# Optimization experiments

Hardware: AMD Instinct MI355X
Metric: run time of the kernel (lower is better)

The kernel has to match this reference:

```python
import jax, jax.numpy as jnp
import numpy as np

B, N, D, H, E, ED = 32, 256, 1024, 16, 512, 256
HD = D // H
NEG = float(np.finfo(np.float32).min)


def setup_inputs() -> dict:
    key = jax.random.key(0)
    ks = iter(jax.random.split(key, 16))
    def nrm(shape, fan_in):
        return jax.random.normal(next(ks), shape, jnp.float32) / np.sqrt(fan_in)
    return {
        "x": jax.random.normal(next(ks), (B, N, D), jnp.float32),
        "node_masks": jnp.ones((B, N), jnp.float32),
        "relation_edges": jax.random.randint(next(ks), (B, E, 2), 0, N, jnp.int64),
        "relation_masks": jnp.ones((B, E), jnp.float32),
        "relation_embeddings": jax.random.normal(next(ks), (B, E, ED), jnp.float32),
        "ln_g": jnp.ones((D,), jnp.float32), "ln_b": jnp.zeros((D,), jnp.float32),
        "Wq": nrm((D, D), D), "bq": jnp.zeros((D,), jnp.float32),
        "Wk": nrm((D, D), D), "bk": jnp.zeros((D,), jnp.float32),
        "Wv": nrm((D, D), D), "bv": jnp.zeros((D,), jnp.float32),
        "We": nrm((ED, H), ED), "be": jnp.zeros((H,), jnp.float32),
        "Wo": nrm((D, D), D), "bo": jnp.zeros((D,), jnp.float32),
        "ff_g": jnp.ones((D,), jnp.float32), "ff_b": jnp.zeros((D,), jnp.float32),
        "W1": nrm((D, 4 * D), D), "b1": jnp.zeros((4 * D,), jnp.float32),
        "W2": nrm((4 * D, D), 4 * D), "b2": jnp.zeros((D,), jnp.float32),
    }


def _ln(x, g, b):
    m = jnp.mean(x, axis=-1, keepdims=True)
    v = jnp.mean((x - m) ** 2, axis=-1, keepdims=True)
    return (x - m) / jnp.sqrt(v + 1e-5) * g + b


def reference(x, node_masks, relation_edges, relation_masks, relation_embeddings,
              ln_g, ln_b, Wq, bq, Wk, bk, Wv, bv, We, be, Wo, bo,
              ff_g, ff_b, W1, b1, W2, b2):
    residual = x
    xn = _ln(x, ln_g, ln_b)
    # [B,N,D] -> [B,H,N,HD]
    def split_heads(t):
        return t.reshape(B, N, H, HD).transpose(0, 2, 1, 3)
    q = split_heads(xn @ Wq + bq)
    k = split_heads(xn @ Wk + bk)
    v = split_heads(xn @ Wv + bv)
    attn = jnp.einsum('bhqd,bhkd->bhqk', q, k) / np.sqrt(HD)

    nb = node_masks.astype(bool)
    pair_mask = nb[:, None, :, None] & nb[:, None, None, :]  # [B,1,N,N]

    # --- scatter edge list into dense adjacency + per-head bias ---
    src = jnp.clip(relation_edges[..., 0], 0, N - 1)  # [B,E]
    dst = jnp.clip(relation_edges[..., 1], 0, N - 1)
    valid = relation_masks.astype(bool)
    # route invalid edges to a padding row/col N, sliced off afterwards
    src_w = jnp.where(valid, src, N)
    dst_w = jnp.where(valid, dst, N)
    b_idx = jnp.broadcast_to(jnp.arange(B)[:, None], (B, E))

    Np = N + 1
    adj = jnp.broadcast_to(jnp.eye(Np, dtype=bool), (B, Np, Np))
    adj = adj.at[b_idx, src_w, dst_w].set(True).at[b_idx, dst_w, src_w].set(True)
    rel_adj = adj[:, :N, :N][:, None]  # [B,1,N,N]

    eb = relation_embeddings @ We + be  # [B,E,H]
    bias = jnp.zeros((B, Np, Np, H), x.dtype)
    bias = bias.at[b_idx, src_w, dst_w].set(eb).at[b_idx, dst_w, src_w].set(eb)
    rel_bias = bias[:, :N, :N, :].transpose(0, 3, 1, 2)  # [B,H,N,N]

    attn = attn + rel_bias
    pair_mask = pair_mask & rel_adj
    attn = jnp.where(pair_mask, attn, NEG)
    attn = jax.nn.softmax(attn, axis=-1)
    attn = jnp.nan_to_num(attn)

    out = jnp.einsum('bhqk,bhkd->bhqd', attn, v).transpose(0, 2, 1, 3).reshape(B, N, D)
    x = residual + (out @ Wo + bo)
    h = _ln(x, ff_g, ff_b)
    h = jax.nn.silu(h @ W1 + b1) @ W2 + b2
    x = x + h
    return x * node_masks[..., None]
```

## Files before the change

kernel.cpp:

```cpp
#include <hip/hip_runtime.h>
#include <math.h>

#define B_  32
#define N_  256
#define D_  1024
#define H_  16
#define E_  512
#define ED_ 256
#define HD_ 64
#define QS_ 3072
#define NEG_ (-3.4028234663852886e38f)

typedef __attribute__((ext_vector_type(8))) short short8;
typedef __attribute__((ext_vector_type(4))) float f32x4;
typedef __attribute__((ext_vector_type(16))) float f32x16;
typedef unsigned short ushort_t;
typedef unsigned int uint_t;

union U16x8 { uint4 u4; ushort_t s[8]; };

static __device__ __forceinline__ ushort_t f2bf(float f) {
    uint_t u = __builtin_bit_cast(uint_t, f);
    u = (u + 0x7fff + ((u >> 16) & 1)) >> 16;
    return (ushort_t)u;
}

static __device__ __forceinline__ void gload_lds16(const void* g, void* l) {
    __builtin_amdgcn_global_load_lds(
        (const __attribute__((address_space(1))) unsigned int*)g,
        (__attribute__((address_space(3))) unsigned int*)l, 16, 0, 0);
}

__global__ __launch_bounds__(256) void ln_bf16_kernel(const float* __restrict__ x,
                                                      const float* __restrict__ g,
                                                      const float* __restrict__ b,
                                                      ushort_t* __restrict__ out) {
    int row = blockIdx.x;
    const float* xr = x + (size_t)row * D_;
    ushort_t* yr = out + (size_t)row * D_;
    __shared__ float red[256];
    int t = threadIdx.x;
    float vals[4];
    float s = 0.f;
#pragma unroll
    for (int i = 0; i < 4; ++i) { vals[i] = xr[t + i * 256]; s += vals[i]; }
    red[t] = s; __syncthreads();
    for (int off = 128; off > 0; off >>= 1) { if (t < off) red[t] += red[t + off]; __syncthreads(); }
    float mean = red[0] * (1.f / D_);
    __syncthreads();
    float vs = 0.f;
#pragma unroll
    for (int i = 0; i < 4; ++i) { float d = vals[i] - mean; vs += d * d; }
    red[t] = vs; __syncthreads();
    for (int off = 128; off > 0; off >>= 1) { if (t < off) red[t] += red[t + off]; __syncthreads(); }
    float rstd = 1.f / sqrtf(red[0] * (1.f / D_) + 1e-5f);
#pragma unroll
    for (int i = 0; i < 4; ++i) {
        int c = t + i * 256;
        yr[c] = f2bf((vals[i] - mean) * rstd * g[c] + b[c]);
    }
}

__global__ __launch_bounds__(256) void prep_kernel(
    const float* __restrict__ Wq, const float* __restrict__ Wk,
    const float* __restrict__ Wv, const float* __restrict__ Wo,
    const float* __restrict__ W1, const float* __restrict__ W2,
    const float* __restrict__ bq, const float* __restrict__ bk,
    const float* __restrict__ bv,
    ushort_t* __restrict__ qkvT, ushort_t* __restrict__ WoT,
    ushort_t* __restrict__ W1T, ushort_t* __restrict__ W2T,
    float* __restrict__ cb)
{
    int id = blockIdx.x;
    if (id >= 12288) {
        int i = (id - 12288) * 256 + threadIdx.x;
        cb[i] = (i < 1024) ? bq[i] : ((i < 2048) ? bk[i - 1024] : bv[i - 2048]);
        return;
    }
    const float* in; ushort_t* outp; int K, N, tid;
    if (id < 4096) {
        int wsel = id >> 10; tid = id & 1023; K = D_; N = D_;
        in   = (wsel == 0) ? Wq : (wsel == 1) ? Wk : (wsel == 2) ? Wv : Wo;
        outp = (wsel == 0) ? qkvT : (wsel == 1) ? qkvT + 1024 * 1024
             : (wsel == 2) ? qkvT + 2 * 1024 * 1024 : WoT;
    } else if (id < 8192) { tid = id - 4096; K = D_; N = 4 * D_; in = W1; outp = W1T; }
    else                  { tid = id - 8192; K = 4 * D_; N = D_; in = W2; outp = W2T; }
    int tilesX = N >> 5;
    int n0 = (tid % tilesX) * 32, k0 = (tid / tilesX) * 32;

    __shared__ float tile[32][33];
    int tx = threadIdx.x & 31, ty = threadIdx.x >> 5;
#pragma unroll
    for (int r = 0; r < 4; ++r)
        tile[ty + r * 8][tx] = in[(size_t)(k0 + ty + r * 8) * N + n0 + tx];
    __syncthreads();
#pragma unroll
    for (int r = 0; r < 4; ++r)
        outp[(size_t)(n0 + ty + r * 8) * K + k0 + tx] = f2bf(tile[tx][ty + r * 8]);
}

__global__ __launch_bounds__(256) void eb_kernel(const float* __restrict__ re,
                                                 const float* __restrict__ We,
                                                 const float* __restrict__ be,
                                                 float* __restrict__ eb) {
    __shared__ float rs[16 * 256];
    __shared__ float wl[256 * 16];
    int t = threadIdx.x;
    int be0 = blockIdx.x * 16;
#pragma unroll
    for (int i = 0; i < 16; ++i) wl[t + i * 256] = We[t + i * 256];
#pragma unroll
    for (int i = 0; i < 16; ++i) rs[t + i * 256] = re[(size_t)be0 * 256 + t + i * 256];
    __syncthreads();
    int el = t >> 4, h = t & 15;
    float s = be[h];
#pragma unroll 8
    for (int i = 0; i < 256; ++i) s += rs[el * 256 + i] * wl[i * 16 + h];
    eb[(size_t)(be0 + el) * 16 + h] = s;
}

__global__ void scatter_kernel(const int* __restrict__ edges, const float* __restrict__ emask,
                               int* __restrict__ prio) {
    int idx = blockIdx.x * blockDim.x + threadIdx.x;
    if (idx >= B_ * E_) return;
    if (emask[idx] == 0.f) return;
    int b = idx / E_, e = idx % E_;
    int s = edges[2 * idx], d = edges[2 * idx + 1];
    s = min(max(s, 0), N_ - 1);
    d = min(max(d, 0), N_ - 1);
    int* base = prio + (size_t)b * N_ * N_;
    atomicMax(&base[s * N_ + d], e);
    atomicMax(&base[d * N_ + s], e + E_);
}

template<int MODE>
__global__ __launch_bounds__(256) void gemm_bf16(
    const ushort_t* __restrict__ A, const ushort_t* __restrict__ BT,
    const float* __restrict__ bias, const float* __restrict__ res,
    const float* __restrict__ nm, void* __restrict__ Cout,
    int M, int N, int K)
{
    __shared__ ushort_t As[128 * 64];
    __shared__ ushort_t Bs[128 * 64];
    int t = threadIdx.x;
    int lane = t & 63;
    int l31 = lane & 31, lh = lane >> 5;
    int w = t >> 6;
    int wr = (w >> 1) * 64, wc = (w & 1) * 64;

    int bid = blockIdx.x;
    int xcd = bid & 7;
    int lid = bid >> 3;
    int st  = lid >> 5;
    int ls  = lid & 31;
    int brow = xcd * 8 + (ls >> 2);
    int bcol = st * 4 + (ls & 3);
    int row0 = brow * 128, col0 = bcol * 128;

    const ushort_t* Ag = A + (size_t)row0 * K;
    const ushort_t* Bg = BT + (size_t)col0 * K;
    int srow = t >> 3;
    int slot = t & 7;
    int sc = (slot ^ (srow & 7)) * 8;

    f32x16 acc[2][2];
#pragma unroll
    for (int i = 0; i < 2; ++i)
#pragma unroll
        for (int j = 0; j < 2; ++j)
#pragma unroll
            for (int r = 0; r < 16; ++r) acc[i][j][r] = 0.f;

    for (int k0 = 0; k0 < K; k0 += 64) {
#pragma unroll
        for (int i = 0; i < 4; ++i) {
            gload_lds16(Ag + (size_t)(i * 32 + srow) * K + k0 + sc, (char*)As + i * 4096 + t * 16);
            gload_lds16(Bg + (size_t)(i * 32 + srow) * K + k0 + sc, (char*)Bs + i * 4096 + t * 16);
        }
        __syncthreads();
#pragma unroll
        for (int ks = 0; ks < 4; ++ks) {
            short8 af[2], bf[2];
#pragma unroll
            for (int it = 0; it < 2; ++it) {
                int m = wr + it * 32 + l31;
                int x = ((ks * 2 + lh) ^ (m & 7)) * 16;
                af[it] = *(const short8*)((const char*)As + m * 128 + x);
            }
#pragma unroll
            for (int jt = 0; jt < 2; ++jt) {
                int n = wc + jt * 32 + l31;
                int x = ((ks * 2 + lh) ^ (n & 7)) * 16;
                bf[jt] = *(const short8*)((const char*)Bs + n * 128 + x);
            }
#pragma unroll
            for (int it = 0; it < 2; ++it)
#pragma unroll
                for (int jt = 0; jt < 2; ++jt)
                    acc[it][jt] = __builtin_amdgcn_mfma_f32_32x32x16_bf16(af[it], bf[jt], acc[it][jt], 0, 0, 0);
        }
        __syncthreads();
    }

#pragma unroll
    for (int it = 0; it < 2; ++it) {
#pragma unroll
        for (int jt = 0; jt < 2; ++jt) {
            int col = col0 + wc + jt * 32 + l31;
            float bcol_b = bias[col];
#pragma unroll
            for (int reg = 0; reg < 16; ++reg) {
                int row = row0 + wr + it * 32 + (reg & 3) + 8 * (reg >> 2) + 4 * lh;
                float v = acc[it][jt][reg] + bcol_b;
                if (MODE == 0) {
                    ((ushort_t*)Cout)[(size_t)row * N + col] = f2bf(v);
                } else if (MODE == 1) {
                    ((float*)Cout)[(size_t)row * N + col] = v + res[(size_t)row * N + col];
                } else if (MODE == 2) {
                    v = v / (1.f + __expf(-v));
                    ((ushort_t*)Cout)[(size_t)row * N + col] = f2bf(v);
                } else {
                    v = (v + res[(size_t)row * N + col]) * nm[row];
                    ((float*)Cout)[(size_t)row * N + col] = v;
                }
            }
        }
    }
}

__global__ __launch_bounds__(256, 2) void attn_mfma_kernel(
    const ushort_t* __restrict__ qkv, const int* __restrict__ prio,
    const float* __restrict__ eb, const float* __restrict__ nm,
    ushort_t* __restrict__ out)
{
    int xb = blockIdx.x;
    int bid = (xb & 7) * 256 + (xb >> 3);
    int h = bid & 15, qt = (bid >> 4) & 3, b = bid >> 6;
    int t = threadIdx.x;

    __shared__ ushort_t Ks[256 * 72];
    __shared__ ushort_t Vt[64 * 264];

    int lane = t & 63, c = lane & 15, quad = lane >> 4;
    int w = t >> 6;
    int qbase = qt * 64 + w * 16 + quad * 4;

    int pr[16][4];
    const int* prp = prio + ((size_t)(b * N_ + qbase)) * N_ + c;
#pragma unroll
    for (int j = 0; j < 16; ++j)
#pragma unroll
        for (int r = 0; r < 4; ++r)
            pr[j][r] = prp[(size_t)r * N_ + j * 16];

    float nmq[4];
#pragma unroll
    for (int r = 0; r < 4; ++r) nmq[r] = nm[b * N_ + qbase + r];
    float nmk[16];
#pragma unroll
    for (int j = 0; j < 16; ++j) nmk[j] = nm[b * N_ + j * 16 + c];

    const ushort_t* qg = qkv + ((size_t)(b * N_ + qt * 64 + w * 16 + c)) * QS_ + h * HD_;
    short8 aq0 = *(const short8*)(const void*)(qg + quad * 8);
    short8 aq1 = *(const short8*)(const void*)(qg + 32 + quad * 8);

    int lr = t >> 3, lc = (t & 7) * 8;
    const ushort_t* kg = qkv + ((size_t)(b * N_)) * QS_ + 1024 + h * HD_;
#pragma unroll
    for (int r = 0; r < 256; r += 32)
        *(uint4*)&Ks[(lr + r) * 72 + lc] = *(const uint4*)&kg[(size_t)(lr + r) * QS_ + lc];
    const ushort_t* vg = qkv + ((size_t)(b * N_)) * QS_ + 2048 + h * HD_;
#pragma unroll
    for (int r = 0; r < 256; r += 32) {
        U16x8 uu; uu.u4 = *(const uint4*)&vg[(size_t)(lr + r) * QS_ + lc];
#pragma unroll
        for (int i = 0; i < 8; ++i)
            Vt[(lc + i) * 264 + lr + r] = uu.s[i];
    }

    const float* ebb = eb + (size_t)b * E_ * H_ + h;
    float badd[16][4];
#pragma unroll
    for (int j = 0; j < 16; ++j) {
        int key = j * 16 + c;
#pragma unroll
        for (int r = 0; r < 4; ++r) {
            int p = pr[j][r];
            float bias = 0.f;
            bool adj = (key == qbase + r);
            if (p >= 0) {
                int e = (p >= E_) ? p - E_ : p;
                bias = ebb[(size_t)e * H_];
                adj = true;
            }
            bool ok = adj && (nmq[r] != 0.f) && (nmk[j] != 0.f);
            badd[j][r] = ok ? bias : -3.0e38f;
        }
    }
    __syncthreads();

    f32x4 z = {0.f, 0.f, 0.f, 0.f};
    f32x4 acc[16];
#pragma unroll
    for (int j = 0; j < 16; ++j) acc[j] = z;
    __builtin_amdgcn_s_setprio(1);
#pragma unroll
    for (int j = 0; j < 16; ++j) {
        short8 b0 = *(const short8*)(const void*)(Ks + (j * 16 + c) * 72 + quad * 8);
        short8 b1 = *(const short8*)(const void*)(Ks + (j * 16 + c) * 72 + 32 + quad * 8);
        acc[j] = __builtin_amdgcn_mfma_f32_16x16x32_bf16(aq0, b0, acc[j], 0, 0, 0);
        acc[j] = __builtin_amdgcn_mfma_f32_16x16x32_bf16(aq1, b1, acc[j], 0, 0, 0);
    }
    __builtin_amdgcn_s_setprio(0);

#pragma unroll
    for (int j = 0; j < 16; ++j)
#pragma unroll
        for (int r = 0; r < 4; ++r)
            acc[j][r] = acc[j][r] * 0.125f + badd[j][r];

    float inv[4];
#pragma unroll
    for (int r = 0; r < 4; ++r) {
        float m = acc[0][r];
#pragma unroll
        for (int j = 1; j < 16; ++j) m = fmaxf(m, acc[j][r]);
        m = fmaxf(m, __shfl_xor(m, 1));
        m = fmaxf(m, __shfl_xor(m, 2));
        m = fmaxf(m, __shfl_xor(m, 4));
        m = fmaxf(m, __shfl_xor(m, 8));
        float s = 0.f;
#pragma unroll
        for (int j = 0; j < 16; ++j) {
            float p = __expf(acc[j][r] - m);
            acc[j][r] = p;
            s += p;
        }
        s += __shfl_xor(s, 1);
        s += __shfl_xor(s, 2);
        s += __shfl_xor(s, 4);
        s += __shfl_xor(s, 8);
        inv[r] = 1.f / s;
    }

    __syncthreads();
    ushort_t* Ps = Ks;
#pragma unroll
    for (int j = 0; j < 16; ++j)
#pragma unroll
        for (int r = 0; r < 4; ++r)
            Ps[(w * 16 + quad * 4 + r) * 264 + j * 16 + c] = f2bf(acc[j][r] * inv[r]);
    asm volatile("s_waitcnt lgkmcnt(0)" ::: "memory");

    f32x4 oc[4];
#pragma unroll
    for (int dt = 0; dt < 4; ++dt) oc[dt] = z;
    __builtin_amdgcn_s_setprio(1);
#pragma unroll
    for (int k0 = 0; k0 < 256; k0 += 32) {
        short8 ap = *(const short8*)(const void*)(Ps + (w * 16 + c) * 264 + k0 + quad * 8);
#pragma unroll
        for (int dt = 0; dt < 4; ++dt) {
            short8 bv = *(const short8*)(const void*)(Vt + (dt * 16 + c) * 264 + k0 + quad * 8);
            oc[dt] = __builtin_amdgcn_mfma_f32_16x16x32_bf16(ap, bv, oc[dt], 0, 0, 0);
        }
    }
    __builtin_amdgcn_s_setprio(0);
    ushort_t* og = out + ((size_t)(b * N_ + qt * 64 + w * 16)) * D_ + h * HD_;
#pragma unroll
    for (int dt = 0; dt < 4; ++dt)
#pragma unroll
        for (int r = 0; r < 4; ++r)
            og[(size_t)(quad * 4 + r) * D_ + dt * 16 + c] = f2bf(oc[dt][r]);
}

extern "C" void kernel_launch(void* const* d_in, const int* in_sizes, int n_in,
                              void* d_out, int out_size, void* d_ws, size_t ws_size,
                              hipStream_t stream) {
    const float* x     = (const float*)d_in[0];
    const float* nm    = (const float*)d_in[1];
    const int*   edges = (const int*)d_in[2];
    const float* emask = (const float*)d_in[3];
    const float* remb  = (const float*)d_in[4];
    const float* ln_g  = (const float*)d_in[5];
    const float* ln_b  = (const float*)d_in[6];
    const float* Wq = (const float*)d_in[7];  const float* bq = (const float*)d_in[8];
    const float* Wk = (const float*)d_in[9];  const float* bk = (const float*)d_in[10];
    const float* Wv = (const float*)d_in[11]; const float* bv = (const float*)d_in[12];
    const float* We = (const float*)d_in[13]; const float* be = (const float*)d_in[14];
    const float* Wo = (const float*)d_in[15]; const float* bo = (const float*)d_in[16];
    const float* ff_g = (const float*)d_in[17]; const float* ff_b = (const float*)d_in[18];
    const float* W1 = (const float*)d_in[19]; const float* b1 = (const float*)d_in[20];
    const float* W2 = (const float*)d_in[21]; const float* b2 = (const float*)d_in[22];
    float* out = (float*)d_out;

    char* ws = (char*)d_ws;
    const size_t MB = 1ll << 20;
    int*      prio = (int*)ws;
    float*    ebuf = (float*)(ws + 8 * MB);
    ushort_t* xn   = (ushort_t*)(ws + 9 * MB);
    float*    x2   = (float*)(ws + 25 * MB);
    ushort_t* hn   = (ushort_t*)(ws + 57 * MB);
    ushort_t* qkv  = (ushort_t*)(ws + 73 * MB);
    ushort_t* mid  = qkv;
    ushort_t* qkvT = (ushort_t*)(ws + 137 * MB);
    ushort_t* WoT  = (ushort_t*)(ws + 143 * MB);
    ushort_t* W1T  = (ushort_t*)(ws + 145 * MB);
    ushort_t* W2T  = (ushort_t*)(ws + 153 * MB);
    float*    cb   = (float*)(ws + 161 * MB);
    ushort_t* aout = xn;

    const int M = B_ * N_;

    (void)hipMemsetAsync(prio, 0xFF, (size_t)B_ * N_ * N_ * sizeof(int), stream);
    eb_kernel<<<B_ * E_ / 16, 256, 0, stream>>>(remb, We, be, ebuf);
    scatter_kernel<<<(B_ * E_ + 255) / 256, 256, 0, stream>>>(edges, emask, prio);

    prep_kernel<<<12300, 256, 0, stream>>>(Wq, Wk, Wv, Wo, W1, W2, bq, bk, bv,
                                           qkvT, WoT, W1T, W2T, cb);

    ln_bf16_kernel<<<M, 256, 0, stream>>>(x, ln_g, ln_b, xn);

    gemm_bf16<0><<<24 * 64, 256, 0, stream>>>(xn, qkvT, cb, nullptr, nullptr, qkv, M, QS_, D_);

    attn_mfma_kernel<<<B_ * H_ * 4, 256, 0, stream>>>(qkv, prio, ebuf, nm, aout);

    gemm_bf16<1><<<8 * 64, 256, 0, stream>>>(aout, WoT, bo, x, nullptr, x2, M, D_, D_);
    ln_bf16_kernel<<<M, 256, 0, stream>>>(x2, ff_g, ff_b, hn);

    gemm_bf16<2><<<32 * 64, 256, 0, stream>>>(hn, W1T, b1, nullptr, nullptr, mid, M, 4 * D_, D_);
    gemm_bf16<3><<<8 * 64, 256, 0, stream>>>(mid, W2T, b2, x2, nm, out, M, D_, 4 * D_);
}
```

Before: 502.7 us.

## Use 128x256 wide-tile GEMM for QKV/FFN1 and deepen K step for N=1024 GEMMs

Adds a gemm_w kernel with 128x256 output tiles (each wave computing 64x128) for the QKV and W1 projections. This raises MFMA work per LDS load and halves the number of blocks. The remaining gemm_bf16 (Wo, W2) now loads two 64-wide K slabs per barrier, which halves the number of sync points. The trade-off is more accumulator registers and more LDS per block, which can lower occupancy.

Result: slower. 555.7 us (+10.6%).

```diff
diff --git a/kernel.cpp b/kernel.cpp
--- a/kernel.cpp
+++ b/kernel.cpp
@@ -133,6 +133,90 @@
     atomicMax(&base[d * N_ + s], e + E_);
 }
 
+template<int MODE, int NBC>
+__global__ __launch_bounds__(256) void gemm_w(
+    const ushort_t* __restrict__ A, const ushort_t* __restrict__ BT,
+    const float* __restrict__ bias, void* __restrict__ Cout,
+    int M, int N, int K)
+{
+    __shared__ ushort_t As[128 * 64];
+    __shared__ ushort_t Bs[256 * 64];
+    int t = threadIdx.x;
+    int lane = t & 63;
+    int l31 = lane & 31, lh = lane >> 5;
+    int w = t >> 6;
+    int wr = (w >> 1) * 64, wc = (w & 1) * 128;
+
+    int bid = blockIdx.x;
+    int xcd = bid & 7;
+    int lid = bid >> 3;
+    int brow = xcd * 8 + lid / NBC;
+    int bcol = lid % NBC;
+    int row0 = brow * 128, col0 = bcol * 256;
+
+    const ushort_t* Ag = A + (size_t)row0 * K;
+    const ushort_t* Bg = BT + (size_t)col0 * K;
+    int srow = t >> 3;
+    int slot = t & 7;
+    int sc = (slot ^ (srow & 7)) * 8;
+
+    f32x16 acc[2][4];
+#pragma unroll
+    for (int i = 0; i < 2; ++i)
+#pragma unroll
+        for (int j = 0; j < 4; ++j)
+#pragma unroll
+            for (int r = 0; r < 16; ++r) acc[i][j][r] = 0.f;
+
+    for (int k0 = 0; k0 < K; k0 += 64) {
+#pragma unroll
+        for (int i = 0; i < 4; ++i)
+            gload_lds16(Ag + (size_t)(i * 32 + srow) * K + k0 + sc, (char*)As + i * 4096 + t * 16);
+#pragma unroll
+        for (int i = 0; i < 8; ++i)
+            gload_lds16(Bg + (size_t)(i * 32 + srow) * K + k0 + sc, (char*)Bs + i * 4096 + t * 16);
+        __syncthreads();
+#pragma unroll
+        for (int ks = 0; ks < 4; ++ks) {
+            short8 af[2], bfr[4];
+#pragma unroll
+            for (int it = 0; it < 2; ++it) {
+                int m = wr + it * 32 + l31;
+                int x = ((ks * 2 + lh) ^ (m & 7)) * 16;
+                af[it] = *(const short8*)((const char*)As + m * 128 + x);
+            }
+#pragma unroll
+            for (int jt = 0; jt < 4; ++jt) {
+                int n = wc + jt * 32 + l31;
+                int x = ((ks * 2 + lh) ^ (n & 7)) * 16;
+                bfr[jt] = *(const short8*)((const char*)Bs + n * 128 + x);
+            }
+#pragma unroll
+            for (int it = 0; it < 2; ++it)
+#pragma unroll
+                for (int jt = 0; jt < 4; ++jt)
+                    acc[it][jt] = __builtin_amdgcn_mfma_f32_32x32x16_bf16(af[it], bfr[jt], acc[it][jt], 0, 0, 0);
+        }
+        __syncthreads();
+    }
+
+#pragma unroll
+    for (int it = 0; it < 2; ++it) {
+#pragma unroll
+        for (int jt = 0; jt < 4; ++jt) {
+            int col = col0 + wc + jt * 32 + l31;
+            float bcol_b = bias[col];
+#pragma unroll
+            for (int reg = 0; reg < 16; ++reg) {
+                int row = row0 + wr + it * 32 + (reg & 3) + 8 * (reg >> 2) + 4 * lh;
+                float v = acc[it][jt][reg] + bcol_b;
+                if (MODE == 2) v = v / (1.f + __expf(-v));
+                ((ushort_t*)Cout)[(size_t)row * N + col] = f2bf(v);
+            }
+        }
+    }
+}
+
 template<int MODE>
 __global__ __launch_bounds__(256) void gemm_bf16(
     const ushort_t* __restrict__ A, const ushort_t* __restrict__ BT,
@@ -140,8 +224,8 @@
     const float* __restrict__ nm, void* __restrict__ Cout,
     int M, int N, int K)
 {
-    __shared__ ushort_t As[128 * 64];
-    __shared__ ushort_t Bs[128 * 64];
+    __shared__ ushort_t As[2][128 * 64];
+    __shared__ ushort_t Bs[2][128 * 64];
     int t = threadIdx.x;
     int lane = t & 63;
     int l31 = lane & 31, lh = lane >> 5;
@@ -171,33 +255,40 @@
 #pragma unroll
             for (int r = 0; r < 16; ++r) acc[i][j][r] = 0.f;
 
-    for (int k0 = 0; k0 < K; k0 += 64) {
-#pragma unroll
-        for (int i = 0; i < 4; ++i) {
-            gload_lds16(Ag + (size_t)(i * 32 + srow) * K + k0 + sc, (char*)As + i * 4096 + t * 16);
-            gload_lds16(Bg + (size_t)(i * 32 + srow) * K + k0 + sc, (char*)Bs + i * 4096 + t * 16);
-        }
+    for (int k0 = 0; k0 < K; k0 += 128) {
+#pragma unroll
+        for (int p = 0; p < 2; ++p)
+#pragma unroll
+            for (int i = 0; i < 4; ++i) {
+                gload_lds16(Ag + (size_t)(i * 32 + srow) * K + k0 + p * 64 + sc,
+                            (char*)As + p * 16384 + i * 4096 + t * 16);
+                gload_lds16(Bg + (size_t)(i * 32 + srow) * K + k0 + p * 64 + sc,
+                            (char*)Bs + p * 16384 + i * 4096 + t * 16);
+            }
         __syncthreads();
 #pragma unroll
-        for (int ks = 0; ks < 4; ++ks) {
-            short8 af[2], bf[2];
+        for (int ks8 = 0; ks8 < 8; ++ks8) {
+            const char* Ab = (const char*)As + (ks8 >> 2) * 16384;
+            const char* Bb = (const char*)Bs + (ks8 >> 2) * 16384;
+            int kk = ks8 & 3;
+            short8 af[2], bfr[2];
 #pragma unroll
             for (int it = 0; it < 2; ++it) {
                 int m = wr + it * 32 + l31;
-                int x = ((ks * 2 + lh) ^ (m & 7)) * 16;
-                af[it] = *(const short8*)((const char*)As + m * 128 + x);
+                int x = ((kk * 2 + lh) ^ (m & 7)) * 16;
+                af[it] = *(const short8*)(Ab + m * 128 + x);
             }
 #pragma unroll
             for (int jt = 0; jt < 2; ++jt) {
                 int n = wc + jt * 32 + l31;
-                int x = ((ks * 2 + lh) ^ (n & 7)) * 16;
-                bf[jt] = *(const short8*)((const char*)Bs + n * 128 + x);
+                int x = ((kk * 2 + lh) ^ (n & 7)) * 16;
+                bfr[jt] = *(const short8*)(Bb + n * 128 + x);
             }
 #pragma unroll
             for (int it = 0; it < 2; ++it)
 #pragma unroll
                 for (int jt = 0; jt < 2; ++jt)
-                    acc[it][jt] = __builtin_amdgcn_mfma_f32_32x32x16_bf16(af[it], bf[jt], acc[it][jt], 0, 0, 0);
+                    acc[it][jt] = __builtin_amdgcn_mfma_f32_32x32x16_bf16(af[it], bfr[jt], acc[it][jt], 0, 0, 0);
         }
         __syncthreads();
     }
@@ -212,13 +303,8 @@
             for (int reg = 0; reg < 16; ++reg) {
                 int row = row0 + wr + it * 32 + (reg & 3) + 8 * (reg >> 2) + 4 * lh;
                 float v = acc[it][jt][reg] + bcol_b;
-                if (MODE == 0) {
-                    ((ushort_t*)Cout)[(size_t)row * N + col] = f2bf(v);
-                } else if (MODE == 1) {
+                if (MODE == 1) {
                     ((float*)Cout)[(size_t)row * N + col] = v + res[(size_t)row * N + col];
-                } else if (MODE == 2) {
-                    v = v / (1.f + __expf(-v));
-                    ((ushort_t*)Cout)[(size_t)row * N + col] = f2bf(v);
                 } else {
                     v = (v + res[(size_t)row * N + col]) * nm[row];
                     ((float*)Cout)[(size_t)row * N + col] = v;
@@ -421,13 +507,13 @@
 
     ln_bf16_kernel<<<M, 256, 0, stream>>>(x, ln_g, ln_b, xn);
 
-    gemm_bf16<0><<<24 * 64, 256, 0, stream>>>(xn, qkvT, cb, nullptr, nullptr, qkv, M, QS_, D_);
+    gemm_w<0, 12><<<768, 256, 0, stream>>>(xn, qkvT, cb, qkv, M, QS_, D_);
 
     attn_mfma_kernel<<<B_ * H_ * 4, 256, 0, stream>>>(qkv, prio, ebuf, nm, aout);
 
     gemm_bf16<1><<<8 * 64, 256, 0, stream>>>(aout, WoT, bo, x, nullptr, x2, M, D_, D_);
     ln_bf16_kernel<<<M, 256, 0, stream>>>(x2, ff_g, ff_b, hn);
 
-    gemm_bf16<2><<<32 * 64, 256, 0, stream>>>(hn, W1T, b1, nullptr, nullptr, mid, M, 4 * D_, D_);
+    gemm_w<2, 16><<<1024, 256, 0, stream>>>(hn, W1T, b1, mid, M, 4 * D_, D_);
     gemm_bf16<3><<<8 * 64, 256, 0, stream>>>(mid, W2T, b2, x2, nm, out, M, D_, 4 * D_);
 }
```
